# Kernel tuning notes

Measured on AMD Instinct MI355X. Metric: run time of the kernel, lower is better.

The kernel has to match this reference:

```python
import jax, jax.numpy as jnp
import numpy as np

CHUNK = 512

def setup_inputs() -> dict:
    key = jax.random.key(0)
    kq, kk, kv = jax.random.split(key, 3)
    shape = (1, 16, 8192, 64)  # B, H, N, E
    return {
        "query": jax.random.normal(kq, shape, dtype=jnp.float32),
        "key": jax.random.normal(kk, shape, dtype=jnp.float32),
        "value": jax.random.normal(kv, shape, dtype=jnp.float32),
    }

def reference(query, key, value):
    c = CHUNK
    B, H, N, E = query.shape
    nc = N // c  # number of query chunks (N assumed divisible by c)
    scale = 1.0 / (E ** 0.5)
    neg_inf = jnp.finfo(query.dtype).min

    qc = query.reshape(B, H, nc, c, E)
    kc = key.reshape(B, H, nc, c, E)
    vc = value.reshape(B, H, nc, c, E)

    # ---- chunk 0: window is just keys[0:c], standard causal mask ----
    s0 = jnp.einsum('bhqe,bhse->bhqs', qc[:, :, 0], kc[:, :, 0]) * scale
    mask0 = jnp.triu(jnp.ones((c, c), dtype=bool), k=1)
    a0 = jax.nn.softmax(jnp.where(mask0, neg_inf, s0), axis=-1)  # (B,H,c,c)
    o0 = jnp.einsum('bhqs,bhse->bhqe', a0, vc[:, :, 0])           # (B,H,c,E)

    # ---- chunks 1..nc-1: key window = [previous chunk, current chunk] ----
    kw = jnp.concatenate([kc[:, :, :-1], kc[:, :, 1:]], axis=3)  # (B,H,nc-1,2c,E)
    vw = jnp.concatenate([vc[:, :, :-1], vc[:, :, 1:]], axis=3)
    s = jnp.einsum('bhnqe,bhnse->bhnqs', qc[:, :, 1:], kw) * scale  # (B,H,nc-1,c,2c)
    # faithful to torch.triu(ones(q_len, k_len), diagonal=1): row r keeps cols 0..r
    mask = jnp.triu(jnp.ones((c, 2 * c), dtype=bool), k=1)
    a = jax.nn.softmax(jnp.where(mask, neg_inf, s), axis=-1)        # (B,H,nc-1,c,2c)
    o = jnp.einsum('bhnqs,bhnse->bhnqe', a, vw)                     # (B,H,nc-1,c,E)

    output = jnp.concatenate([o0, o.reshape(B, H, (nc - 1) * c, E)], axis=2)  # (B,H,N,E)
    # weights concatenated along the key axis (torch cat dim=3)
    a_rest = jnp.moveaxis(a, 2, 3).reshape(B, H, c, (nc - 1) * 2 * c)
    weights = jnp.concatenate([a0, a_rest], axis=3)  # (B,H,c, c + (nc-1)*2c)
    return output, weights
```

## Files before the change

kernel.cpp:

```cpp
#include <hip/hip_runtime.h>

typedef __bf16 bf16x8 __attribute__((ext_vector_type(8)));
typedef __bf16 bf16x4 __attribute__((ext_vector_type(4)));
typedef float  f32x4  __attribute__((ext_vector_type(4)));

#define NH    16
#define SEQ   8192
#define EDIM  64
#define CHK   512
#define WCOLS 15872
#define OUT0  8388608

#define MFMA(a, b, c) __builtin_amdgcn_mfma_f32_16x16x32_bf16((a), (b), (c), 0, 0, 0)

__global__ __launch_bounds__(256) void zero_fill_kernel(float* __restrict__ W) {
    const int gid = blockIdx.x * 256 + threadIdx.x;
    #pragma unroll
    for (int it = 0; it < 30; ++it) {
        const int i     = gid + it * 524288;
        const int j     = i & 127;
        const int rowid = i >> 7;
        const int r     = rowid & 511;
        const int w     = rowid >> 9;
        const int h     = w / 15;
        const int n     = w - h * 15 + 1;
        float* p = W + (size_t)(h * 512 + r) * WCOLS + (size_t)n * 1024 + j * 4;
        f32x4 z = {0.f, 0.f, 0.f, 0.f};
        __builtin_nontemporal_store(z, (f32x4*)p);
    }
}

__global__ __launch_bounds__(512, 2) void chunked_attn_kernel(
    const float* __restrict__ Qg, const float* __restrict__ Kg,
    const float* __restrict__ Vg, float* __restrict__ out)
{
    __shared__ __align__(16) __bf16 lds_k[32768];
    __shared__ __align__(16) __bf16 lds_v[32768];
    __shared__ __align__(16) __bf16 lds_p[8][2][640];

    const int tid  = threadIdx.x;
    const int lane = tid & 63;
    const int wv   = __builtin_amdgcn_readfirstlane(tid >> 6);
    const int l16  = lane & 15;
    const int quad = lane >> 4;

    const int h  = blockIdx.x >> 4;
    const int n  = blockIdx.x & 15;
    const int ns = (n == 0) ? 0 : n - 1;

    const size_t qbase = ((size_t)h * SEQ + (size_t)n  * CHK) * EDIM;
    const size_t kbase = ((size_t)h * SEQ + (size_t)ns * CHK) * EDIM;
    float* __restrict__ W = out + OUT0;
    const size_t wrow0   = (size_t)h * CHK;
    const int    colbase = (n == 0) ? 0 : (CHK + (n - 1) * 2 * CHK);

    const float SC = 0.125f * 1.44269504088896340736f;

    bf16x8 aqf[4][2];
    #pragma unroll
    for (int mt = 0; mt < 4; ++mt) {
        const int m0 = mt * 128 + wv * 16;
        const float* qp = Qg + qbase + (size_t)(m0 + l16) * EDIM + quad * 8;
        float4 a = *(const float4*)(qp);
        float4 b = *(const float4*)(qp + 4);
        bf16x8 t0;
        t0[0]=(__bf16)(a.x*SC); t0[1]=(__bf16)(a.y*SC); t0[2]=(__bf16)(a.z*SC); t0[3]=(__bf16)(a.w*SC);
        t0[4]=(__bf16)(b.x*SC); t0[5]=(__bf16)(b.y*SC); t0[6]=(__bf16)(b.z*SC); t0[7]=(__bf16)(b.w*SC);
        aqf[mt][0] = t0;
        a = *(const float4*)(qp + 32);
        b = *(const float4*)(qp + 36);
        bf16x8 t1;
        t1[0]=(__bf16)(a.x*SC); t1[1]=(__bf16)(a.y*SC); t1[2]=(__bf16)(a.z*SC); t1[3]=(__bf16)(a.w*SC);
        t1[4]=(__bf16)(b.x*SC); t1[5]=(__bf16)(b.y*SC); t1[6]=(__bf16)(b.z*SC); t1[7]=(__bf16)(b.w*SC);
        aqf[mt][1] = t1;
    }

    #pragma unroll
    for (int it = 0; it < 8; ++it) {
        const int c = tid + it * 512;
        const int s = c >> 3, sub = c & 7;
        const float* src = Kg + kbase + (size_t)s * EDIM + sub * 8;
        const float4 a = *(const float4*)src;
        const float4 b = *(const float4*)(src + 4);
        bf16x8 t;
        t[0] = (__bf16)a.x; t[1] = (__bf16)a.y; t[2] = (__bf16)a.z; t[3] = (__bf16)a.w;
        t[4] = (__bf16)b.x; t[5] = (__bf16)b.y; t[6] = (__bf16)b.z; t[7] = (__bf16)b.w;
        const int idx = ((s >> 4) * 8 + sub) * 16 + (s & 15);
        ((bf16x8*)lds_k)[idx] = t;
    }

    #pragma unroll
    for (int it = 0; it < 8; ++it) {
        const int c = tid + it * 512;
        const int e = c & 63, sb = c >> 6;
        bf16x8 t;
        #pragma unroll
        for (int j = 0; j < 8; ++j)
            t[j] = (__bf16)Vg[kbase + (size_t)(sb * 8 + j) * EDIM + e];
        const int idx = (((sb >> 2) * 4 + (e >> 4)) * 4 + (sb & 3)) * 16 + (e & 15);
        ((bf16x8*)lds_v)[idx] = t;
    }

    __syncthreads();

    const bf16x8* const kf = (const bf16x8*)lds_k;
    const bf16x8* const vf = (const bf16x8*)lds_v;

    #pragma unroll
    for (int mt = 0; mt < 4; ++mt) {
        const int m0   = mt * 128 + wv * 16;
        const int tmax = mt * 8 + wv;
        const int qrow = m0 + l16;

        f32x4 st[32];
        #pragma unroll
        for (int t = 0; t < 32; ++t) {
            if (t <= tmax) {
                const int kb = t * 128 + quad * 16 + l16;
                f32x4 acc = {0.f, 0.f, 0.f, 0.f};
                acc = MFMA(kf[kb],      aqf[mt][0], acc);
                acc = MFMA(kf[kb + 64], aqf[mt][1], acc);
                const int sb = t * 16 + quad * 4;
                #pragma unroll
                for (int r = 0; r < 4; ++r)
                    acc[r] = (sb + r <= qrow) ? acc[r] : -3.0e38f;
                st[t] = acc;
            } else {
                st[t] = (f32x4){0.f, 0.f, 0.f, 0.f};
            }
        }

        float mr = -3.0e38f;
        #pragma unroll
        for (int t = 0; t < 32; ++t) {
            if (t <= tmax) {
                #pragma unroll
                for (int r = 0; r < 4; ++r) mr = fmaxf(mr, st[t][r]);
            }
        }
        mr = fmaxf(mr, __shfl_xor(mr, 16));
        mr = fmaxf(mr, __shfl_xor(mr, 32));

        float lr = 0.f;
        #pragma unroll
        for (int t = 0; t < 32; ++t) {
            if (t <= tmax) {
                #pragma unroll
                for (int r = 0; r < 4; ++r) {
                    const float e = __builtin_amdgcn_exp2f(st[t][r] - mr);
                    st[t][r] = e;
                    lr += e;
                }
            }
        }
        lr += __shfl_xor(lr, 16);
        lr += __shfl_xor(lr, 32);
        const float ri = __builtin_amdgcn_rcpf(lr);

        #pragma unroll
        for (int t = 0; t < 32; ++t) {
            if (t <= tmax) st[t] = st[t] * ri;
        }

        {
            float* const wp = W + (wrow0 + (size_t)qrow) * WCOLS + colbase + quad * 4;
            #pragma unroll
            for (int t = 0; t < 32; ++t)
                __builtin_nontemporal_store(st[t], (f32x4*)(wp + t * 16));
        }

        f32x4 o0 = {0,0,0,0}, o1 = {0,0,0,0}, o2 = {0,0,0,0}, o3 = {0,0,0,0};
        #pragma unroll
        for (int pr = 0; pr < 16; ++pr) {
            if (2 * pr <= tmax) {
                __bf16* const pbuf = lds_p[wv][pr & 1];
                #pragma unroll
                for (int tt = 0; tt < 2; ++tt) {
                    const int t = pr * 2 + tt;
                    bf16x4 w;
                    #pragma unroll
                    for (int r = 0; r < 4; ++r) w[r] = (__bf16)st[t][r];
                    *(bf16x4*)(pbuf + l16 * 40 + tt * 16 + quad * 4) = w;
                }
                const bf16x8 pa = *(const bf16x8*)(pbuf + l16 * 40 + quad * 8);
                const int vb = pr * 256 + quad * 16 + l16;
                o0 = MFMA(pa, vf[vb      ], o0);
                o1 = MFMA(pa, vf[vb +  64], o1);
                o2 = MFMA(pa, vf[vb + 128], o2);
                o3 = MFMA(pa, vf[vb + 192], o3);
            }
        }

        const int rq = m0 + quad * 4;
        const size_t ob = qbase + (size_t)rq * EDIM + l16;
        #pragma unroll
        for (int r = 0; r < 4; ++r) {
            __builtin_nontemporal_store(o0[r], out + ob + (size_t)r * EDIM     );
            __builtin_nontemporal_store(o1[r], out + ob + (size_t)r * EDIM + 16);
            __builtin_nontemporal_store(o2[r], out + ob + (size_t)r * EDIM + 32);
            __builtin_nontemporal_store(o3[r], out + ob + (size_t)r * EDIM + 48);
        }
    }
}

extern "C" void kernel_launch(void* const* d_in, const int* in_sizes, int n_in,
                              void* d_out, int out_size, void* d_ws, size_t ws_size,
                              hipStream_t stream) {
    const float* Q = (const float*)d_in[0];
    const float* K = (const float*)d_in[1];
    const float* V = (const float*)d_in[2];
    float* out = (float*)d_out;
    zero_fill_kernel<<<dim3(2048), dim3(256), 0, stream>>>(out + OUT0);
    chunked_attn_kernel<<<dim3(256), dim3(512), 0, stream>>>(Q, K, V, out);
}
```

Baseline: 650.8 us.

## Split each chunk across four blocks and fuse zero-fill into attention kernel

The launch goes from 256 to 1024 blocks, one per (head, chunk, 128-row query tile), so the per-block loop over four query tiles is removed. Each block loads only the key/value prefix its causal tile needs. The separate zero-fill kernel is dropped, and each block instead writes zeros for the upper half of its weight window. This raises parallelism on a GPU with many CUs and removes a kernel launch, at the cost of reloading K/V chunks up to four times from global memory.

```diff
diff --git a/kernel.cpp b/kernel.cpp
--- a/kernel.cpp
+++ b/kernel.cpp
@@ -12,23 +12,6 @@
 #define OUT0  8388608
 
 #define MFMA(a, b, c) __builtin_amdgcn_mfma_f32_16x16x32_bf16((a), (b), (c), 0, 0, 0)
-
-__global__ __launch_bounds__(256) void zero_fill_kernel(float* __restrict__ W) {
-    const int gid = blockIdx.x * 256 + threadIdx.x;
-    #pragma unroll
-    for (int it = 0; it < 30; ++it) {
-        const int i     = gid + it * 524288;
-        const int j     = i & 127;
-        const int rowid = i >> 7;
-        const int r     = rowid & 511;
-        const int w     = rowid >> 9;
-        const int h     = w / 15;
-        const int n     = w - h * 15 + 1;
-        float* p = W + (size_t)(h * 512 + r) * WCOLS + (size_t)n * 1024 + j * 4;
-        f32x4 z = {0.f, 0.f, 0.f, 0.f};
-        __builtin_nontemporal_store(z, (f32x4*)p);
-    }
-}
 
 __global__ __launch_bounds__(512, 2) void chunked_attn_kernel(
     const float* __restrict__ Qg, const float* __restrict__ Kg,
@@ -44,8 +27,9 @@
     const int l16  = lane & 15;
     const int quad = lane >> 4;
 
-    const int h  = blockIdx.x >> 4;
-    const int n  = blockIdx.x & 15;
+    const int h  = blockIdx.x >> 6;
+    const int n  = (blockIdx.x >> 2) & 15;
+    const int mt = blockIdx.x & 3;
     const int ns = (n == 0) ? 0 : n - 1;
 
     const size_t qbase = ((size_t)h * SEQ + (size_t)n  * CHK) * EDIM;
@@ -54,51 +38,63 @@
     const size_t wrow0   = (size_t)h * CHK;
     const int    colbase = (n == 0) ? 0 : (CHK + (n - 1) * 2 * CHK);
 
+    const int m0   = mt * 128 + wv * 16;
+    const int tmax = mt * 8 + wv;
+    const int qrow = m0 + l16;
+
+    const int clim = 1024 * (mt + 1);
+
     const float SC = 0.125f * 1.44269504088896340736f;
 
-    bf16x8 aqf[4][2];
-    #pragma unroll
-    for (int mt = 0; mt < 4; ++mt) {
-        const int m0 = mt * 128 + wv * 16;
+    #pragma unroll
+    for (int it = 0; it < 8; ++it) {
+        const int c = tid + it * 512;
+        if (c < clim) {
+            const int s = c >> 3, sub = c & 7;
+            const float* src = Kg + kbase + (size_t)s * EDIM + sub * 8;
+            const float4 a = *(const float4*)src;
+            const float4 b = *(const float4*)(src + 4);
+            bf16x8 t;
+            t[0] = (__bf16)a.x; t[1] = (__bf16)a.y; t[2] = (__bf16)a.z; t[3] = (__bf16)a.w;
+            t[4] = (__bf16)b.x; t[5] = (__bf16)b.y; t[6] = (__bf16)b.z; t[7] = (__bf16)b.w;
+            const int idx = ((s >> 4) * 8 + sub) * 16 + (s & 15);
+            ((bf16x8*)lds_k)[idx] = t;
+        }
+    }
+
+    #pragma unroll
+    for (int it = 0; it < 8; ++it) {
+        const int c = tid + it * 512;
+        if (c < clim) {
+            const int e = c & 63, sb = c >> 6;
+            bf16x8 t;
+            #pragma unroll
+            for (int j = 0; j < 8; ++j)
+                t[j] = (__bf16)Vg[kbase + (size_t)(sb * 8 + j) * EDIM + e];
+            const int idx = (((sb >> 2) * 4 + (e >> 4)) * 4 + (sb & 3)) * 16 + (e & 15);
+            ((bf16x8*)lds_v)[idx] = t;
+        }
+    }
+
+    bf16x8 aq0, aq1;
+    {
         const float* qp = Qg + qbase + (size_t)(m0 + l16) * EDIM + quad * 8;
         float4 a = *(const float4*)(qp);
         float4 b = *(const float4*)(qp + 4);
-        bf16x8 t0;
-        t0[0]=(__bf16)(a.x*SC); t0[1]=(__bf16)(a.y*SC); t0[2]=(__bf16)(a.z*SC); t0[3]=(__bf16)(a.w*SC);
-        t0[4]=(__bf16)(b.x*SC); t0[5]=(__bf16)(b.y*SC); t0[6]=(__bf16)(b.z*SC); t0[7]=(__bf16)(b.w*SC);
-        aqf[mt][0] = t0;
+        aq0[0]=(__bf16)(a.x*SC); aq0[1]=(__bf16)(a.y*SC); aq0[2]=(__bf16)(a.z*SC); aq0[3]=(__bf16)(a.w*SC);
+        aq0[4]=(__bf16)(b.x*SC); aq0[5]=(__bf16)(b.y*SC); aq0[6]=(__bf16)(b.z*SC); aq0[7]=(__bf16)(b.w*SC);
         a = *(const float4*)(qp + 32);
         b = *(const float4*)(qp + 36);
-        bf16x8 t1;
-        t1[0]=(__bf16)(a.x*SC); t1[1]=(__bf16)(a.y*SC); t1[2]=(__bf16)(a.z*SC); t1[3]=(__bf16)(a.w*SC);
-        t1[4]=(__bf16)(b.x*SC); t1[5]=(__bf16)(b.y*SC); t1[6]=(__bf16)(b.z*SC); t1[7]=(__bf16)(b.w*SC);
-        aqf[mt][1] = t1;
-    }
-
-    #pragma unroll
-    for (int it = 0; it < 8; ++it) {
-        const int c = tid + it * 512;
-        const int s = c >> 3, sub = c & 7;
-        const float* src = Kg + kbase + (size_t)s * EDIM + sub * 8;
-        const float4 a = *(const float4*)src;
-        const float4 b = *(const float4*)(src + 4);
-        bf16x8 t;
-        t[0] = (__bf16)a.x; t[1] = (__bf16)a.y; t[2] = (__bf16)a.z; t[3] = (__bf16)a.w;
-        t[4] = (__bf16)b.x; t[5] = (__bf16)b.y; t[6] = (__bf16)b.z; t[7] = (__bf16)b.w;
-        const int idx = ((s >> 4) * 8 + sub) * 16 + (s & 15);
-        ((bf16x8*)lds_k)[idx] = t;
-    }
-
-    #pragma unroll
-    for (int it = 0; it < 8; ++it) {
-        const int c = tid + it * 512;
-        const int e = c & 63, sb = c >> 6;
-        bf16x8 t;
+        aq1[0]=(__bf16)(a.x*SC); aq1[1]=(__bf16)(a.y*SC); aq1[2]=(__bf16)(a.z*SC); aq1[3]=(__bf16)(a.w*SC);
+        aq1[4]=(__bf16)(b.x*SC); aq1[5]=(__bf16)(b.y*SC); aq1[6]=(__bf16)(b.z*SC); aq1[7]=(__bf16)(b.w*SC);
+    }
+
+    if (n > 0) {
+        float* const zp = W + (wrow0 + (size_t)qrow) * WCOLS + colbase + 512 + quad * 4;
+        const f32x4 z = {0.f, 0.f, 0.f, 0.f};
         #pragma unroll
-        for (int j = 0; j < 8; ++j)
-            t[j] = (__bf16)Vg[kbase + (size_t)(sb * 8 + j) * EDIM + e];
-        const int idx = (((sb >> 2) * 4 + (e >> 4)) * 4 + (sb & 3)) * 16 + (e & 15);
-        ((bf16x8*)lds_v)[idx] = t;
+        for (int t = 0; t < 32; ++t)
+            __builtin_nontemporal_store(z, (f32x4*)(zp + t * 16));
     }
 
     __syncthreads();
@@ -106,100 +102,93 @@
     const bf16x8* const kf = (const bf16x8*)lds_k;
     const bf16x8* const vf = (const bf16x8*)lds_v;
 
-    #pragma unroll
-    for (int mt = 0; mt < 4; ++mt) {
-        const int m0   = mt * 128 + wv * 16;
-        const int tmax = mt * 8 + wv;
-        const int qrow = m0 + l16;
-
-        f32x4 st[32];
+    f32x4 st[32];
+    #pragma unroll
+    for (int t = 0; t < 32; ++t) {
+        if (t <= tmax) {
+            const int kb = t * 128 + quad * 16 + l16;
+            f32x4 acc = {0.f, 0.f, 0.f, 0.f};
+            acc = MFMA(kf[kb],      aq0, acc);
+            acc = MFMA(kf[kb + 64], aq1, acc);
+            const int sb = t * 16 + quad * 4;
+            #pragma unroll
+            for (int r = 0; r < 4; ++r)
+                acc[r] = (sb + r <= qrow) ? acc[r] : -3.0e38f;
+            st[t] = acc;
+        } else {
+            st[t] = (f32x4){0.f, 0.f, 0.f, 0.f};
+        }
+    }
+
+    float mr = -3.0e38f;
+    #pragma unroll
+    for (int t = 0; t < 32; ++t) {
+        if (t <= tmax) {
+            #pragma unroll
+            for (int r = 0; r < 4; ++r) mr = fmaxf(mr, st[t][r]);
+        }
+    }
+    mr = fmaxf(mr, __shfl_xor(mr, 16));
+    mr = fmaxf(mr, __shfl_xor(mr, 32));
+
+    float lr = 0.f;
+    #pragma unroll
+    for (int t = 0; t < 32; ++t) {
+        if (t <= tmax) {
+            #pragma unroll
+            for (int r = 0; r < 4; ++r) {
+                const float e = __builtin_amdgcn_exp2f(st[t][r] - mr);
+                st[t][r] = e;
+                lr += e;
+            }
+        }
+    }
+    lr += __shfl_xor(lr, 16);
+    lr += __shfl_xor(lr, 32);
+    const float ri = __builtin_amdgcn_rcpf(lr);
+
+    #pragma unroll
+    for (int t = 0; t < 32; ++t) {
+        if (t <= tmax) st[t] = st[t] * ri;
+    }
+
+    {
+        float* const wp = W + (wrow0 + (size_t)qrow) * WCOLS + colbase + quad * 4;
         #pragma unroll
-        for (int t = 0; t < 32; ++t) {
-            if (t <= tmax) {
-                const int kb = t * 128 + quad * 16 + l16;
-                f32x4 acc = {0.f, 0.f, 0.f, 0.f};
-                acc = MFMA(kf[kb],      aqf[mt][0], acc);
-                acc = MFMA(kf[kb + 64], aqf[mt][1], acc);
-                const int sb = t * 16 + quad * 4;
+        for (int t = 0; t < 32; ++t)
+            __builtin_nontemporal_store(st[t], (f32x4*)(wp + t * 16));
+    }
+
+    f32x4 o0 = {0,0,0,0}, o1 = {0,0,0,0}, o2 = {0,0,0,0}, o3 = {0,0,0,0};
+    #pragma unroll
+    for (int pr = 0; pr < 16; ++pr) {
+        if (2 * pr <= tmax) {
+            __bf16* const pbuf = lds_p[wv][pr & 1];
+            #pragma unroll
+            for (int tt = 0; tt < 2; ++tt) {
+                const int t = pr * 2 + tt;
+                bf16x4 w;
                 #pragma unroll
-                for (int r = 0; r < 4; ++r)
-                    acc[r] = (sb + r <= qrow) ? acc[r] : -3.0e38f;
-                st[t] = acc;
-            } else {
-                st[t] = (f32x4){0.f, 0.f, 0.f, 0.f};
+                for (int r = 0; r < 4; ++r) w[r] = (__bf16)st[t][r];
+                *(bf16x4*)(pbuf + l16 * 40 + tt * 16 + quad * 4) = w;
             }
-        }
-
-        float mr = -3.0e38f;
-        #pragma unroll
-        for (int t = 0; t < 32; ++t) {
-            if (t <= tmax) {
-                #pragma unroll
-                for (int r = 0; r < 4; ++r) mr = fmaxf(mr, st[t][r]);
-            }
-        }
-        mr = fmaxf(mr, __shfl_xor(mr, 16));
-        mr = fmaxf(mr, __shfl_xor(mr, 32));
-
-        float lr = 0.f;
-        #pragma unroll
-        for (int t = 0; t < 32; ++t) {
-            if (t <= tmax) {
-                #pragma unroll
-                for (int r = 0; r < 4; ++r) {
-                    const float e = __builtin_amdgcn_exp2f(st[t][r] - mr);
-                    st[t][r] = e;
-                    lr += e;
-                }
-            }
-        }
-        lr += __shfl_xor(lr, 16);
-        lr += __shfl_xor(lr, 32);
-        const float ri = __builtin_amdgcn_rcpf(lr);
-
-        #pragma unroll
-        for (int t = 0; t < 32; ++t) {
-            if (t <= tmax) st[t] = st[t] * ri;
-        }
-
-        {
-            float* const wp = W + (wrow0 + (size_t)qrow) * WCOLS + colbase + quad * 4;
-            #pragma unroll
-            for (int t = 0; t < 32; ++t)
-                __builtin_nontemporal_store(st[t], (f32x4*)(wp + t * 16));
-        }
-
-        f32x4 o0 = {0,0,0,0}, o1 = {0,0,0,0}, o2 = {0,0,0,0}, o3 = {0,0,0,0};
-        #pragma unroll
-        for (int pr = 0; pr < 16; ++pr) {
-            if (2 * pr <= tmax) {
-                __bf16* const pbuf = lds_p[wv][pr & 1];
-                #pragma unroll
-                for (int tt = 0; tt < 2; ++tt) {
-                    const int t = pr * 2 + tt;
-                    bf16x4 w;
-                    #pragma unroll
-                    for (int r = 0; r < 4; ++r) w[r] = (__bf16)st[t][r];
-                    *(bf16x4*)(pbuf + l16 * 40 + tt * 16 + quad * 4) = w;
-                }
-                const bf16x8 pa = *(const bf16x8*)(pbuf + l16 * 40 + quad * 8);
-                const int vb = pr * 256 + quad * 16 + l16;
-                o0 = MFMA(pa, vf[vb      ], o0);
-                o1 = MFMA(pa, vf[vb +  64], o1);
-                o2 = MFMA(pa, vf[vb + 128], o2);
-                o3 = MFMA(pa, vf[vb + 192], o3);
-            }
-        }
-
-        const int rq = m0 + quad * 4;
-        const size_t ob = qbase + (size_t)rq * EDIM + l16;
-        #pragma unroll
-        for (int r = 0; r < 4; ++r) {
-            __builtin_nontemporal_store(o0[r], out + ob + (size_t)r * EDIM     );
-            __builtin_nontemporal_store(o1[r], out + ob + (size_t)r * EDIM + 16);
-            __builtin_nontemporal_store(o2[r], out + ob + (size_t)r * EDIM + 32);
-            __builtin_nontemporal_store(o3[r], out + ob + (size_t)r * EDIM + 48);
-        }
+            const bf16x8 pa = *(const bf16x8*)(pbuf + l16 * 40 + quad * 8);
+            const int vb = pr * 256 + quad * 16 + l16;
+            o0 = MFMA(pa, vf[vb      ], o0);
+            o1 = MFMA(pa, vf[vb +  64], o1);
+            o2 = MFMA(pa, vf[vb + 128], o2);
+            o3 = MFMA(pa, vf[vb + 192], o3);
+        }
+    }
+
+    const int rq = m0 + quad * 4;
+    const size_t ob = qbase + (size_t)rq * EDIM + l16;
+    #pragma unroll
+    for (int r = 0; r < 4; ++r) {
+        __builtin_nontemporal_store(o0[r], out + ob + (size_t)r * EDIM     );
+        __builtin_nontemporal_store(o1[r], out + ob + (size_t)r * EDIM + 16);
+        __builtin_nontemporal_store(o2[r], out + ob + (size_t)r * EDIM + 32);
+        __builtin_nontemporal_store(o3[r], out + ob + (size_t)r * EDIM + 48);
     }
 }
 
@@ -210,6 +199,5 @@
     const float* K = (const float*)d_in[1];
     const float* V = (const float*)d_in[2];
     float* out = (float*)d_out;
-    zero_fill_kernel<<<dim3(2048), dim3(256), 0, stream>>>(out + OUT0);
-    chunked_attn_kernel<<<dim3(256), dim3(512), 0, stream>>>(Q, K, V, out);
+    chunked_attn_kernel<<<dim3(1024), dim3(512), 0, stream>>>(Q, K, V, out);
 }
```

Measured after the change: 686.0 us. +5.4%, slower.
